# Optimization experiments

Measured on AMD Instinct MI355X. Metric: run time of the kernel, lower is better.

## Reference

```python
import jax, jax.numpy as jnp
import numpy as np

N_BINS = 15
SHARPNESS = 20.0
EPS = 1e-8


def setup_inputs() -> dict:
    key = jax.random.key(0)
    k1, k2 = jax.random.split(key)
    logits = jax.random.normal(k1, (32768, 1000), dtype=jnp.float32)
    labels = jax.random.randint(k2, (32768,), 0, 1000, dtype=jnp.int64)
    return {"logits": logits, "labels": labels}


def reference(logits, labels):
    # softmax over classes, then max-prob confidence and argmax prediction
    probs = jax.nn.softmax(logits, axis=-1)            # [B, C]
    confidences = jnp.max(probs, axis=-1)              # [B]
    predictions = jnp.argmax(probs, axis=-1)           # [B]
    correct = (predictions == labels).astype(confidences.dtype)  # [B]

    bin_boundaries = jnp.linspace(0.0, 1.0, N_BINS + 1, dtype=confidences.dtype)
    bin_lowers = bin_boundaries[:-1][:, None]          # [n_bins, 1]
    bin_uppers = bin_boundaries[1:][:, None]           # [n_bins, 1]

    # soft bin membership, vectorized over bins: [n_bins, B]
    in_bin = (jax.nn.sigmoid(SHARPNESS * (confidences[None, :] - bin_lowers))
              * jax.nn.sigmoid(SHARPNESS * (bin_uppers - confidences[None, :])))

    bin_mass = jnp.sum(in_bin, axis=1)                           # [n_bins]
    bin_accuracy = (in_bin @ correct) / (bin_mass + EPS)         # [n_bins]
    bin_confidence = (in_bin @ confidences) / (bin_mass + EPS)   # [n_bins]

    # sigmoid products are strictly positive so the torch `if in_bin.sum() > 0`
    # branch is always taken; the unconditional sum is equivalent.
    calibration_loss = jnp.sum((bin_accuracy - bin_confidence) ** 2 * bin_mass)
    return calibration_loss / logits.shape[0]
```

## Files before the change

### kernel.cpp

```cpp
#include <hip/hip_runtime.h>
#include <math.h>

#define NBINS 15
#define NBLK  2048
#define WPB   4
#define NWAVES (NBLK * WPB)

__global__ __launch_bounds__(256, 8) void fused_row_bin_kernel(
    const float* __restrict__ logits, const int* __restrict__ labels,
    float* __restrict__ partials, int B)
{
    const int lane = threadIdx.x & 63;
    const int wid  = threadIdx.x >> 6;

    const int   tsel = lane / 15;
    const int   jb   = lane - tsel * 15;
    const float lo   = (float)( jb      * (1.0 / 15.0));
    const float up   = (float)((jb + 1) * (1.0 / 15.0));

    float acc = 0.0f;
    const float NI = -INFINITY;

    for (int row = blockIdx.x * WPB + wid; row < B; row += NWAVES) {
        const float4* rp = reinterpret_cast<const float4*>(logits + (size_t)row * 1000);
        float4 v0 = rp[lane];
        float4 v1 = rp[lane + 64];
        float4 v2 = rp[lane + 128];
        float4 v3 = make_float4(NI, NI, NI, NI);
        if (lane < 58) v3 = rp[lane + 192];
        const int lab = labels[row];

        float t0 = fmaxf(fmaxf(v0.x, v0.y), v0.z);
        float t1 = fmaxf(fmaxf(v0.w, v1.x), v1.y);
        float t2 = fmaxf(fmaxf(v1.z, v1.w), v2.x);
        float t3 = fmaxf(fmaxf(v2.y, v2.z), v2.w);
        float t4 = fmaxf(fmaxf(v3.x, v3.y), v3.z);
        float m  = fmaxf(fmaxf(fmaxf(t0, t1), fmaxf(t2, t3)), fmaxf(t4, v3.w));

        #pragma unroll
        for (int off = 1; off < 64; off <<= 1)
            m = fmaxf(m, __shfl_xor(m, off, 64));

        unsigned long long b00 = __ballot(v0.x == m), b01 = __ballot(v0.y == m);
        unsigned long long b02 = __ballot(v0.z == m), b03 = __ballot(v0.w == m);
        unsigned long long b10 = __ballot(v1.x == m), b11 = __ballot(v1.y == m);
        unsigned long long b12 = __ballot(v1.z == m), b13 = __ballot(v1.w == m);
        unsigned long long b20 = __ballot(v2.x == m), b21 = __ballot(v2.y == m);
        unsigned long long b22 = __ballot(v2.z == m), b23 = __ballot(v2.w == m);
        unsigned long long b30 = __ballot(v3.x == m), b31 = __ballot(v3.y == m);
        unsigned long long b32 = __ballot(v3.z == m), b33 = __ballot(v3.w == m);

        int best = 1 << 30;
        {
            unsigned long long u3 = b30 | b31 | b32 | b33;
            if (u3) {
                int l = __ffsll(u3) - 1;
                int c = ((b30 >> l) & 1) ? 0 : ((b31 >> l) & 1) ? 1 : ((b32 >> l) & 1) ? 2 : 3;
                best = 256 * 3 + 4 * l + c;
            }
            unsigned long long u2 = b20 | b21 | b22 | b23;
            if (u2) {
                int l = __ffsll(u2) - 1;
                int c = ((b20 >> l) & 1) ? 0 : ((b21 >> l) & 1) ? 1 : ((b22 >> l) & 1) ? 2 : 3;
                best = 256 * 2 + 4 * l + c;
            }
            unsigned long long u1 = b10 | b11 | b12 | b13;
            if (u1) {
                int l = __ffsll(u1) - 1;
                int c = ((b10 >> l) & 1) ? 0 : ((b11 >> l) & 1) ? 1 : ((b12 >> l) & 1) ? 2 : 3;
                best = 256 * 1 + 4 * l + c;
            }
            unsigned long long u0 = b00 | b01 | b02 | b03;
            if (u0) {
                int l = __ffsll(u0) - 1;
                int c = ((b00 >> l) & 1) ? 0 : ((b01 >> l) & 1) ? 1 : ((b02 >> l) & 1) ? 2 : 3;
                best = 4 * l + c;
            }
        }
        const float corr = (best == lab) ? 1.0f : 0.0f;

        float s = __expf(v0.x - m) + __expf(v0.y - m) + __expf(v0.z - m) + __expf(v0.w - m)
                + __expf(v1.x - m) + __expf(v1.y - m) + __expf(v1.z - m) + __expf(v1.w - m)
                + __expf(v2.x - m) + __expf(v2.y - m) + __expf(v2.z - m) + __expf(v2.w - m)
                + __expf(v3.x - m) + __expf(v3.y - m) + __expf(v3.z - m) + __expf(v3.w - m);
        #pragma unroll
        for (int off = 1; off < 64; off <<= 1) s += __shfl_xor(s, off, 64);

        const float conf = 1.0f / s;

        if (lane < 45) {
            const float s1 = 1.0f / (1.0f + __expf(-20.0f * (conf - lo)));
            const float s2 = 1.0f / (1.0f + __expf(-20.0f * (up - conf)));
            const float ib = s1 * s2;
            const float wgt = (tsel == 0) ? 1.0f : ((tsel == 1) ? corr : conf);
            acc += ib * wgt;
        }
    }

    __shared__ float part[WPB][48];
    if (lane < 45) part[wid][lane] = acc;
    __syncthreads();
    const int tid = threadIdx.x;
    if (tid < 45) {
        partials[(size_t)tid * NBLK + blockIdx.x] =
            ((part[0][tid] + part[1][tid]) + part[2][tid]) + part[3][tid];
    }
}

__global__ __launch_bounds__(512) void finalize_kernel(
    const float* __restrict__ partials, float* __restrict__ out, int B)
{
    const int tid  = threadIdx.x;
    const int lane = tid & 63;
    const int wid  = tid >> 6;

    __shared__ double dsum[45];
    for (int j = wid; j < 45; j += 8) {
        const float4* fp = reinterpret_cast<const float4*>(partials + (size_t)j * NBLK);
        double s = 0.0;
        #pragma unroll
        for (int t = 0; t < NBLK / 256; ++t) {
            float4 v = fp[lane + 64 * t];
            s += (double)v.x; s += (double)v.y; s += (double)v.z; s += (double)v.w;
        }
        #pragma unroll
        for (int off = 1; off < 64; off <<= 1) s += __shfl_xor(s, off, 64);
        if (lane == 0) dsum[j] = s;
    }
    __syncthreads();

    __shared__ double term[NBINS];
    if (tid < NBINS) {
        const double mass = dsum[tid];
        const double accd = dsum[NBINS + tid]     / (mass + 1e-8);
        const double cfd  = dsum[2 * NBINS + tid] / (mass + 1e-8);
        const double d    = accd - cfd;
        term[tid] = d * d * mass;
    }
    __syncthreads();

    if (tid == 0) {
        double loss = 0.0;
        for (int i = 0; i < NBINS; ++i) loss += term[i];
        out[0] = (float)(loss / (double)B);
    }
}

extern "C" void kernel_launch(void* const* d_in, const int* in_sizes, int n_in,
                              void* d_out, int out_size, void* d_ws, size_t ws_size,
                              hipStream_t stream)
{
    const float* logits = (const float*)d_in[0];
    const int*   labels = (const int*)d_in[1];
    const int B = in_sizes[1];

    float* partials = (float*)d_ws;

    fused_row_bin_kernel<<<NBLK, 256, 0, stream>>>(logits, labels, partials, B);
    finalize_kernel<<<1, 512, 0, stream>>>(partials, (float*)d_out, B);
}
```

Measured before the change: 32.05 us.

## Prefetch next row into LDS via global_load_lds to overlap with compute

Each wave now stages its logits row into a per-wave LDS buffer using asynchronous global-to-LDS loads. It issues the next row's loads right after reading the current row out of LDS, so memory latency overlaps with the softmax, argmax and binning math. This costs 16KB of LDS per block, which may limit occupancy, and adds explicit waitcnt synchronization. Out-of-range lanes in the last chunk load a dummy element and are masked to -inf afterward.

New measurement: 33.08 us. 3.2% more time.

```diff
diff --git a/kernel.cpp b/kernel.cpp
--- a/kernel.cpp
+++ b/kernel.cpp
@@ -5,6 +5,20 @@
 #define NBLK  2048
 #define WPB   4
 #define NWAVES (NBLK * WPB)
+
+#define GLOAD_LDS(gp, lp)                                                  \
+    __builtin_amdgcn_global_load_lds(                                      \
+        (__attribute__((address_space(1))) void*)(gp),                     \
+        (__attribute__((address_space(3))) void*)(lp), 16, 0, 0)
+
+#define STAGE_ROW(r) do {                                                  \
+    const float4* rp_ = reinterpret_cast<const float4*>(                   \
+        logits + (size_t)(r) * 1000);                                      \
+    GLOAD_LDS(rp_ + lane,                            myb);                 \
+    GLOAD_LDS(rp_ + lane + 64,                       myb + 256);           \
+    GLOAD_LDS(rp_ + lane + 128,                      myb + 512);           \
+    GLOAD_LDS(rp_ + ((lane < 58) ? lane + 192 : 0),  myb + 768);           \
+} while (0)
 
 __global__ __launch_bounds__(256, 8) void fused_row_bin_kernel(
     const float* __restrict__ logits, const int* __restrict__ labels,
@@ -21,14 +35,28 @@
     float acc = 0.0f;
     const float NI = -INFINITY;
 
-    for (int row = blockIdx.x * WPB + wid; row < B; row += NWAVES) {
-        const float4* rp = reinterpret_cast<const float4*>(logits + (size_t)row * 1000);
-        float4 v0 = rp[lane];
-        float4 v1 = rp[lane + 64];
-        float4 v2 = rp[lane + 128];
-        float4 v3 = make_float4(NI, NI, NI, NI);
-        if (lane < 58) v3 = rp[lane + 192];
-        const int lab = labels[row];
+    __shared__ float lbuf[WPB][1024];
+    float* myb = &lbuf[wid][0];
+
+    int row = blockIdx.x * WPB + wid;
+    int lab = 0;
+    if (row < B) { STAGE_ROW(row); lab = labels[row]; }
+
+    while (row < B) {
+        const int nrow = row + NWAVES;
+
+        asm volatile("s_waitcnt vmcnt(0)" ::: "memory");
+        const float4* bp = reinterpret_cast<const float4*>(myb);
+        float4 v0 = bp[lane];
+        float4 v1 = bp[lane + 64];
+        float4 v2 = bp[lane + 128];
+        float4 v3 = bp[lane + 192];
+        asm volatile("s_waitcnt lgkmcnt(0)" ::: "memory");
+
+        int nlab = 0;
+        if (nrow < B) { STAGE_ROW(nrow); nlab = labels[nrow]; }
+
+        if (lane >= 58) v3 = make_float4(NI, NI, NI, NI);
 
         float t0 = fmaxf(fmaxf(v0.x, v0.y), v0.z);
         float t1 = fmaxf(fmaxf(v0.w, v1.x), v1.y);
@@ -95,6 +123,8 @@
             const float wgt = (tsel == 0) ? 1.0f : ((tsel == 1) ? corr : conf);
             acc += ib * wgt;
         }
+
+        row = nrow; lab = nlab;
     }
 
     __shared__ float part[WPB][48];
```
